# Kernel tuning notes

Hardware: AMD Instinct MI355X
Metric: run time of the kernel (lower is better)

## Reference

```python
import jax, jax.numpy as jnp
import numpy as np

N, D, IN, OUT, K = 50000, 16, 256, 128, 4  # nodes, sampled degree, input_size, output_size, heads
LEAKY_SLOPE = 0.01  # torch F.leaky_relu default


def setup_inputs() -> dict:
    key = jax.random.key(0)
    k1, k2, k3, k4 = jax.random.split(key, 4)
    X = jax.random.normal(k1, (N, IN), dtype=jnp.float32)
    W = jax.random.normal(k2, (K, OUT, IN), dtype=jnp.float32) * 0.05
    a = jax.random.normal(k3, (K, 2 * OUT), dtype=jnp.float32) * 0.05
    neighbor_idx = jax.random.randint(k4, (N, D), 0, N)  # fixed-degree neighbor sample
    return {"X": X, "W": W, "a": a, "neighbor_idx": neighbor_idx}


def reference(X, W, a, neighbor_idx):
    # X: [N, IN]; W: [K, OUT, IN]; a: [K, 2*OUT]; neighbor_idx: [N, D]
    out_dim = W.shape[1]
    # Per-head linear map of every node once: Wh[k, n] = W[k] @ X[n]
    Wh = jnp.einsum('koi,ni->kno', W, X)                       # [K, N, OUT]
    # a splits: first OUT weights multiply mapped neighbour, second OUT multiply mapped self
    a_nb, a_self = a[:, :out_dim], a[:, out_dim:]
    e_nb = jnp.einsum('kno,ko->kn', Wh, a_nb)                  # [K, N] score contribution as a neighbour
    e_self = jnp.einsum('kno,ko->kn', Wh, a_self)              # [K, N] score contribution as center node
    # Edge logits: e[k, i, d] = leaky_relu(a_nb.Wh[j] + a_self.Wh[i]), j = neighbor_idx[i, d]
    e = jax.nn.leaky_relu(e_nb[:, neighbor_idx] + e_self[:, :, None], LEAKY_SLOPE)  # [K, N, D]
    alpha = jax.nn.softmax(e, axis=-1)                         # softmax over each node's neighbour set
    Wh_nb = jnp.take(Wh, neighbor_idx, axis=1)                 # [K, N, D, OUT] gathered neighbour features
    h = jnp.einsum('knd,kndo->kno', alpha, Wh_nb)              # [K, N, OUT] attention-weighted aggregate
    # Concatenate heads along feature dim, matching per-node head-concat in the torch loop
    return jnp.transpose(h, (1, 0, 2)).reshape(X.shape[0], -1)  # [N, K*OUT]
```

## Files before the change

kernel.cpp:

```cpp
#include <hip/hip_runtime.h>

#define N_NODES 50000
#define D_NB 16
#define IN_DIM 256
#define OUT_DIM 128
#define K_HEADS 4
#define SLOPE 0.01f
#define NSLICE 16
#define SLICE_COLS 32

typedef __attribute__((ext_vector_type(8))) short short8;
typedef __attribute__((ext_vector_type(4))) float f32x4;

static __device__ __forceinline__ unsigned f2bf(float f) {
    unsigned u = __float_as_uint(f);
    unsigned r = u + 0x7fffu + ((u >> 16) & 1u);
    return r >> 16;
}
static __device__ __forceinline__ float bf2f(unsigned short b) {
    return __uint_as_float(((unsigned)b) << 16);
}

__global__ __launch_bounds__(256) void prep_w_kernel(
    const float* __restrict__ W, const float* __restrict__ a,
    unsigned short* __restrict__ Wb, float* __restrict__ wt8)
{
    if (blockIdx.x < 2048) {
        const int id = blockIdx.x * 256 + threadIdx.x;
        Wb[id] = (unsigned short)f2bf(W[id]);
        return;
    }
    const int v = blockIdx.x - 2048;
    const int k = v >> 1, s = v & 1;
    const int i = threadIdx.x;
    const float* av = a + k * 2 * OUT_DIM + s * OUT_DIM;
    float acc = 0.f;
    #pragma unroll 4
    for (int o = 0; o < OUT_DIM; ++o)
        acc += W[((size_t)k * OUT_DIM + o) * IN_DIM + i] * av[o];
    wt8[v * IN_DIM + i] = acc;
}

__global__ __launch_bounds__(256) void prep_kernel(
    const float* __restrict__ X, const float* __restrict__ wt8,
    unsigned short* __restrict__ Xb, float* __restrict__ e_nb4, float* __restrict__ e_self4)
{
    const int t = threadIdx.x;
    const int w = t >> 6;
    const int lane = t & 63;
    const int n = blockIdx.x * 4 + w;

    const f32x4 x = __builtin_nontemporal_load(
        (const f32x4*)(X + (size_t)n * IN_DIM + lane * 4));
    uint2 pk;
    pk.x = f2bf(x[0]) | (f2bf(x[1]) << 16);
    pk.y = f2bf(x[2]) | (f2bf(x[3]) << 16);
    *(uint2*)(Xb + (size_t)n * IN_DIM + lane * 4) = pk;

    float p[8];
    #pragma unroll
    for (int v = 0; v < 8; ++v) {
        const float4 wv = *(const float4*)(wt8 + v * IN_DIM + lane * 4);
        p[v] = x[0] * wv.x + x[1] * wv.y + x[2] * wv.z + x[3] * wv.w;
    }
    #pragma unroll
    for (int sh = 32; sh >= 1; sh >>= 1) {
        #pragma unroll
        for (int v = 0; v < 8; ++v) p[v] += __shfl_xor(p[v], sh);
    }
    if (lane == 0) {
        *(float4*)(e_nb4 + (size_t)n * 4)   = float4{p[0], p[2], p[4], p[6]};
        *(float4*)(e_self4 + (size_t)n * 4) = float4{p[1], p[3], p[5], p[7]};
    }
}

__global__ __launch_bounds__(256) void agg_kernel(
    const int* __restrict__ nidx, const unsigned short* __restrict__ Xb,
    const float* __restrict__ e_nb4, const float* __restrict__ e_self4,
    unsigned short* __restrict__ aggX, int n0, int nc)
{
    const int t = threadIdx.x;
    const int w = t >> 6;
    const int lane = t & 63;
    const int n = n0 + blockIdx.x * 4 + w;
    if (n >= n0 + nc || n >= N_NODES) return;

    const int k = lane >> 4;
    const int dl = lane & 15;

    const int nbr = __builtin_nontemporal_load(nidx + (size_t)n * D_NB + dl);
    const float4 eb4 = *(const float4*)(e_nb4 + (size_t)nbr * 4);
    const float4 es4 = *(const float4*)(e_self4 + (size_t)n * 4);
    const float en = (k & 2) ? ((k & 1) ? eb4.w : eb4.z) : ((k & 1) ? eb4.y : eb4.x);
    const float es = (k & 2) ? ((k & 1) ? es4.w : es4.z) : ((k & 1) ? es4.y : es4.x);
    const float xv = en + es;
    const float v = xv > 0.f ? xv : SLOPE * xv;
    float m = v;
    #pragma unroll
    for (int sh = 8; sh >= 1; sh >>= 1) m = fmaxf(m, __shfl_xor(m, sh, 16));
    const float pz = __expf(v - m);
    float sum = pz;
    #pragma unroll
    for (int sh = 8; sh >= 1; sh >>= 1) sum += __shfl_xor(sum, sh, 16);
    const float alpha = pz / sum;

    float acc[4][4] = {};
    #pragma unroll
    for (int h = 0; h < 2; ++h) {
        uint2 u[8];
        #pragma unroll
        for (int b = 0; b < 8; ++b) {
            const int nd = __shfl(nbr, h * 8 + b);
            u[b] = *(const uint2*)(Xb + (size_t)nd * IN_DIM + lane * 4);
        }
        #pragma unroll
        for (int b = 0; b < 8; ++b) {
            const float x0 = bf2f((unsigned short)(u[b].x & 0xffffu));
            const float x1 = bf2f((unsigned short)(u[b].x >> 16));
            const float x2 = bf2f((unsigned short)(u[b].y & 0xffffu));
            const float x3 = bf2f((unsigned short)(u[b].y >> 16));
            #pragma unroll
            for (int kk = 0; kk < 4; ++kk) {
                const float ad = __shfl(alpha, kk * 16 + h * 8 + b);
                acc[kk][0] += ad * x0;
                acc[kk][1] += ad * x1;
                acc[kk][2] += ad * x2;
                acc[kk][3] += ad * x3;
            }
        }
    }
    #pragma unroll
    for (int kk = 0; kk < 4; ++kk) {
        uint2 pk;
        pk.x = f2bf(acc[kk][0]) | (f2bf(acc[kk][1]) << 16);
        pk.y = f2bf(acc[kk][2]) | (f2bf(acc[kk][3]) << 16);
        *(uint2*)(aggX + ((size_t)kk * nc + (n - n0)) * IN_DIM + lane * 4) = pk;
    }
}

__global__ __launch_bounds__(512) void gemm2_kernel(
    const unsigned short* __restrict__ aggX, const unsigned short* __restrict__ Wb,
    float* __restrict__ out, int n0, int nc)
{
    __shared__ unsigned short Wlds[2][SLICE_COLS * IN_DIM];

    const int t = threadIdx.x;
    const int lane = t & 63;
    const int w = t >> 6;
    const int lrow = lane & 15;
    const int lk = lane >> 4;
    const int m0 = n0 + blockIdx.x * 256 + w * 16;

    const int arow0 = m0 + lrow;
    const int arow1 = arow0 + 128;
    const bool av0 = (arow0 < n0 + nc) && (arow0 < N_NODES);
    const bool av1 = (arow1 < n0 + nc) && (arow1 < N_NODES);

    auto STAGE = [&](int st, int buf) {
        const unsigned short* WbS = Wb + (size_t)st * SLICE_COLS * IN_DIM;
        #pragma unroll
        for (int i = 0; i < 2; ++i) {
            const int c = i * 512 + t;
            const int r = c >> 5;
            const int p = c & 31;
            const int cu = p ^ (r & 7);
            const unsigned short* gsrc = WbS + r * IN_DIM + cu * 8;
            unsigned short* ldst = &Wlds[buf][c * 8];
            __builtin_amdgcn_global_load_lds(
                (const __attribute__((address_space(1))) void*)gsrc,
                (__attribute__((address_space(3))) void*)ldst, 16, 0, 0);
        }
    };

    short8 af0[8], af1[8];
    auto LOADAF = [&](int head) {
        const size_t hb = (size_t)head * nc;
        const unsigned short* Ar0 = aggX + (hb + (arow0 - n0)) * IN_DIM + lk * 8;
        const unsigned short* Ar1 = aggX + (hb + (arow1 - n0)) * IN_DIM + lk * 8;
        #pragma unroll
        for (int kk = 0; kk < 8; ++kk) {
            af0[kk] = av0 ? *(const short8*)(Ar0 + kk * 32) : short8{0,0,0,0,0,0,0,0};
            af1[kk] = av1 ? *(const short8*)(Ar1 + kk * 32) : short8{0,0,0,0,0,0,0,0};
        }
    };

    STAGE(0, 0);
    LOADAF(0);
    __syncthreads();

    for (int st = 0; st < NSLICE; ++st) {
        const int buf = st & 1;
        if (st + 1 < NSLICE) STAGE(st + 1, buf ^ 1);
        if ((st & 3) == 0 && st) LOADAF(st >> 2);

        f32x4 acc0[2] = {}, acc1[2] = {};
        #pragma unroll
        for (int kk = 0; kk < 8; ++kk) {
            #pragma unroll
            for (int nt = 0; nt < 2; ++nt) {
                const int row = nt * 16 + lrow;
                const int pos = (kk * 4 + lk) ^ (row & 7);
                const short8 bf = *(const short8*)(&Wlds[buf][row * IN_DIM + pos * 8]);
                acc0[nt] = __builtin_amdgcn_mfma_f32_16x16x32_bf16(bf, af0[kk], acc0[nt], 0, 0, 0);
                acc1[nt] = __builtin_amdgcn_mfma_f32_16x16x32_bf16(bf, af1[kk], acc1[nt], 0, 0, 0);
            }
        }

        const int k = st >> 2, cb = st & 3;
        const size_t cbase = (size_t)k * OUT_DIM + cb * SLICE_COLS + lk * 4;
        #pragma unroll
        for (int nt = 0; nt < 2; ++nt) {
            if (av0) *(f32x4*)(out + (size_t)arow0 * (K_HEADS * OUT_DIM) + cbase + nt * 16) = acc0[nt];
            if (av1) *(f32x4*)(out + (size_t)arow1 * (K_HEADS * OUT_DIM) + cbase + nt * 16) = acc1[nt];
        }
        __syncthreads();
    }
}

extern "C" void kernel_launch(void* const* d_in, const int* in_sizes, int n_in,
                              void* d_out, int out_size, void* d_ws, size_t ws_size,
                              hipStream_t stream) {
    const float* X = (const float*)d_in[0];
    const float* W = (const float*)d_in[1];
    const float* a = (const float*)d_in[2];
    const int* nidx = (const int*)d_in[3];
    float* out = (float*)d_out;

    const size_t WbB  = (size_t)K_HEADS * OUT_DIM * IN_DIM * 2;
    const size_t XbB  = (size_t)N_NODES * IN_DIM * 2;
    const size_t wt8B = (size_t)8 * IN_DIM * 4;
    const size_t eB   = (size_t)K_HEADS * N_NODES * 4;
    auto need = [&](int nc) {
        return WbB + XbB + wt8B + 2 * eB + (size_t)K_HEADS * nc * IN_DIM * 2 + 1024;
    };

    int np, nc;
    if      (ws_size >= need(50000)) { np = 1; nc = 50000; }
    else if (ws_size >= need(25000)) { np = 2; nc = 25000; }
    else                             { np = 4; nc = 12500; }

    char* p = (char*)d_ws;
    unsigned short* Wb   = (unsigned short*)p;   p += WbB;
    unsigned short* Xb   = (unsigned short*)p;   p += XbB;
    float*          wt8  = (float*)p;            p += wt8B;
    float*          enb4 = (float*)p;            p += eB;
    float*          esf4 = (float*)p;            p += eB;
    unsigned short* aggX = (unsigned short*)p;

    hipLaunchKernelGGL(prep_w_kernel, dim3(2056), dim3(256), 0, stream, W, a, Wb, wt8);

    hipLaunchKernelGGL(prep_kernel,
        dim3(N_NODES / 4), dim3(256), 0, stream, X, wt8, Xb, enb4, esf4);

    for (int pass = 0; pass < np; ++pass) {
        const int nb0 = pass * nc;
        hipLaunchKernelGGL(agg_kernel,
            dim3((nc + 3) / 4), dim3(256), 0, stream, nidx, Xb, enb4, esf4, aggX, nb0, nc);
        hipLaunchKernelGGL(gemm2_kernel,
            dim3((nc + 255) / 256), dim3(512), 0, stream, aggX, Wb, out, nb0, nc);
    }
}
```

Measured before the change: 159.9 us.

## Fuse neighbor aggregation and per-head GEMM into one kernel via LDS tile

Merges the aggregation kernel and the GEMM kernel into a single kernel. Each block aggregates 16 nodes for all heads into a swizzled LDS tile, then runs MFMA against the bf16 weights read directly from global memory. This removes the aggX round trip through global memory, the extra kernel launch and the multi-pass workspace logic. In exchange, each block re-reads the full W slice from global memory/L2, and the agg phase and GEMM phase are serialized within a block with a barrier between them.

```diff
diff --git a/kernel.cpp b/kernel.cpp
--- a/kernel.cpp
+++ b/kernel.cpp
@@ -6,8 +6,7 @@
 #define OUT_DIM 128
 #define K_HEADS 4
 #define SLOPE 0.01f
-#define NSLICE 16
-#define SLICE_COLS 32
+#define BN 16
 
 typedef __attribute__((ext_vector_type(8))) short short8;
 typedef __attribute__((ext_vector_type(4))) float f32x4;
@@ -74,146 +73,102 @@
     }
 }
 
-__global__ __launch_bounds__(256) void agg_kernel(
+__global__ __launch_bounds__(512) void fused_kernel(
     const int* __restrict__ nidx, const unsigned short* __restrict__ Xb,
     const float* __restrict__ e_nb4, const float* __restrict__ e_self4,
-    unsigned short* __restrict__ aggX, int n0, int nc)
+    const unsigned short* __restrict__ Wb, float* __restrict__ out)
 {
+    __shared__ unsigned short tile[K_HEADS * BN * IN_DIM];
+
     const int t = threadIdx.x;
     const int w = t >> 6;
     const int lane = t & 63;
-    const int n = n0 + blockIdx.x * 4 + w;
-    if (n >= n0 + nc || n >= N_NODES) return;
+    const int bn0 = blockIdx.x * BN;
 
     const int k = lane >> 4;
     const int dl = lane & 15;
 
-    const int nbr = __builtin_nontemporal_load(nidx + (size_t)n * D_NB + dl);
-    const float4 eb4 = *(const float4*)(e_nb4 + (size_t)nbr * 4);
-    const float4 es4 = *(const float4*)(e_self4 + (size_t)n * 4);
-    const float en = (k & 2) ? ((k & 1) ? eb4.w : eb4.z) : ((k & 1) ? eb4.y : eb4.x);
-    const float es = (k & 2) ? ((k & 1) ? es4.w : es4.z) : ((k & 1) ? es4.y : es4.x);
-    const float xv = en + es;
-    const float v = xv > 0.f ? xv : SLOPE * xv;
-    float m = v;
     #pragma unroll
-    for (int sh = 8; sh >= 1; sh >>= 1) m = fmaxf(m, __shfl_xor(m, sh, 16));
-    const float pz = __expf(v - m);
-    float sum = pz;
-    #pragma unroll
-    for (int sh = 8; sh >= 1; sh >>= 1) sum += __shfl_xor(sum, sh, 16);
-    const float alpha = pz / sum;
+    for (int half = 0; half < 2; ++half) {
+        const int row = 2 * w + half;
+        const int n = bn0 + row;
 
-    float acc[4][4] = {};
-    #pragma unroll
-    for (int h = 0; h < 2; ++h) {
-        uint2 u[8];
+        const int nbr = __builtin_nontemporal_load(nidx + (size_t)n * D_NB + dl);
+        const float4 eb4 = *(const float4*)(e_nb4 + (size_t)nbr * 4);
+        const float4 es4 = *(const float4*)(e_self4 + (size_t)n * 4);
+        const float en = (k & 2) ? ((k & 1) ? eb4.w : eb4.z) : ((k & 1) ? eb4.y : eb4.x);
+        const float es = (k & 2) ? ((k & 1) ? es4.w : es4.z) : ((k & 1) ? es4.y : es4.x);
+        const float xv = en + es;
+        const float v = xv > 0.f ? xv : SLOPE * xv;
+        float m = v;
         #pragma unroll
-        for (int b = 0; b < 8; ++b) {
-            const int nd = __shfl(nbr, h * 8 + b);
-            u[b] = *(const uint2*)(Xb + (size_t)nd * IN_DIM + lane * 4);
+        for (int sh = 8; sh >= 1; sh >>= 1) m = fmaxf(m, __shfl_xor(m, sh, 16));
+        const float pz = __expf(v - m);
+        float sum = pz;
+        #pragma unroll
+        for (int sh = 8; sh >= 1; sh >>= 1) sum += __shfl_xor(sum, sh, 16);
+        const float alpha = pz / sum;
+
+        float acc[4][4] = {};
+        #pragma unroll
+        for (int h2 = 0; h2 < 2; ++h2) {
+            uint2 u[8];
+            #pragma unroll
+            for (int b = 0; b < 8; ++b) {
+                const int nd = __shfl(nbr, h2 * 8 + b);
+                u[b] = *(const uint2*)(Xb + (size_t)nd * IN_DIM + lane * 4);
+            }
+            #pragma unroll
+            for (int b = 0; b < 8; ++b) {
+                const float x0 = bf2f((unsigned short)(u[b].x & 0xffffu));
+                const float x1 = bf2f((unsigned short)(u[b].x >> 16));
+                const float x2 = bf2f((unsigned short)(u[b].y & 0xffffu));
+                const float x3 = bf2f((unsigned short)(u[b].y >> 16));
+                #pragma unroll
+                for (int kk = 0; kk < 4; ++kk) {
+                    const float ad = __shfl(alpha, kk * 16 + h2 * 8 + b);
+                    acc[kk][0] += ad * x0;
+                    acc[kk][1] += ad * x1;
+                    acc[kk][2] += ad * x2;
+                    acc[kk][3] += ad * x3;
+                }
+            }
         }
         #pragma unroll
-        for (int b = 0; b < 8; ++b) {
-            const float x0 = bf2f((unsigned short)(u[b].x & 0xffffu));
-            const float x1 = bf2f((unsigned short)(u[b].x >> 16));
-            const float x2 = bf2f((unsigned short)(u[b].y & 0xffffu));
-            const float x3 = bf2f((unsigned short)(u[b].y >> 16));
-            #pragma unroll
-            for (int kk = 0; kk < 4; ++kk) {
-                const float ad = __shfl(alpha, kk * 16 + h * 8 + b);
-                acc[kk][0] += ad * x0;
-                acc[kk][1] += ad * x1;
-                acc[kk][2] += ad * x2;
-                acc[kk][3] += ad * x3;
-            }
+        for (int kk = 0; kk < 4; ++kk) {
+            uint2 pk;
+            pk.x = f2bf(acc[kk][0]) | (f2bf(acc[kk][1]) << 16);
+            pk.y = f2bf(acc[kk][2]) | (f2bf(acc[kk][3]) << 16);
+            const int boff = (kk * (BN * IN_DIM * 2) + row * (IN_DIM * 2) + lane * 8)
+                             ^ ((row & 7) << 4);
+            *(uint2*)((char*)tile + boff) = pk;
+        }
+    }
+    __syncthreads();
+
+    const int h = w >> 1;
+    const int c4 = (w & 1) * 4;
+    const int lrow = lane & 15;
+    const int lk = lane >> 4;
+
+    f32x4 acc2[4] = {};
+    #pragma unroll
+    for (int kk = 0; kk < 8; ++kk) {
+        const int aoff = (h * (BN * IN_DIM * 2) + lrow * (IN_DIM * 2) + kk * 64 + lk * 16)
+                         ^ ((lrow & 7) << 4);
+        const short8 af = *(const short8*)((const char*)tile + aoff);
+        #pragma unroll
+        for (int c = 0; c < 4; ++c) {
+            const int ocol = (c4 + c) * 16 + lrow;
+            const short8 bf = *(const short8*)(
+                Wb + ((size_t)h * OUT_DIM + ocol) * IN_DIM + kk * 32 + lk * 8);
+            acc2[c] = __builtin_amdgcn_mfma_f32_16x16x32_bf16(bf, af, acc2[c], 0, 0, 0);
         }
     }
     #pragma unroll
-    for (int kk = 0; kk < 4; ++kk) {
-        uint2 pk;
-        pk.x = f2bf(acc[kk][0]) | (f2bf(acc[kk][1]) << 16);
-        pk.y = f2bf(acc[kk][2]) | (f2bf(acc[kk][3]) << 16);
-        *(uint2*)(aggX + ((size_t)kk * nc + (n - n0)) * IN_DIM + lane * 4) = pk;
-    }
-}
-
-__global__ __launch_bounds__(512) void gemm2_kernel(
-    const unsigned short* __restrict__ aggX, const unsigned short* __restrict__ Wb,
-    float* __restrict__ out, int n0, int nc)
-{
-    __shared__ unsigned short Wlds[2][SLICE_COLS * IN_DIM];
-
-    const int t = threadIdx.x;
-    const int lane = t & 63;
-    const int w = t >> 6;
-    const int lrow = lane & 15;
-    const int lk = lane >> 4;
-    const int m0 = n0 + blockIdx.x * 256 + w * 16;
-
-    const int arow0 = m0 + lrow;
-    const int arow1 = arow0 + 128;
-    const bool av0 = (arow0 < n0 + nc) && (arow0 < N_NODES);
-    const bool av1 = (arow1 < n0 + nc) && (arow1 < N_NODES);
-
-    auto STAGE = [&](int st, int buf) {
-        const unsigned short* WbS = Wb + (size_t)st * SLICE_COLS * IN_DIM;
-        #pragma unroll
-        for (int i = 0; i < 2; ++i) {
-            const int c = i * 512 + t;
-            const int r = c >> 5;
-            const int p = c & 31;
-            const int cu = p ^ (r & 7);
-            const unsigned short* gsrc = WbS + r * IN_DIM + cu * 8;
-            unsigned short* ldst = &Wlds[buf][c * 8];
-            __builtin_amdgcn_global_load_lds(
-                (const __attribute__((address_space(1))) void*)gsrc,
-                (__attribute__((address_space(3))) void*)ldst, 16, 0, 0);
-        }
-    };
-
-    short8 af0[8], af1[8];
-    auto LOADAF = [&](int head) {
-        const size_t hb = (size_t)head * nc;
-        const unsigned short* Ar0 = aggX + (hb + (arow0 - n0)) * IN_DIM + lk * 8;
-        const unsigned short* Ar1 = aggX + (hb + (arow1 - n0)) * IN_DIM + lk * 8;
-        #pragma unroll
-        for (int kk = 0; kk < 8; ++kk) {
-            af0[kk] = av0 ? *(const short8*)(Ar0 + kk * 32) : short8{0,0,0,0,0,0,0,0};
-            af1[kk] = av1 ? *(const short8*)(Ar1 + kk * 32) : short8{0,0,0,0,0,0,0,0};
-        }
-    };
-
-    STAGE(0, 0);
-    LOADAF(0);
-    __syncthreads();
-
-    for (int st = 0; st < NSLICE; ++st) {
-        const int buf = st & 1;
-        if (st + 1 < NSLICE) STAGE(st + 1, buf ^ 1);
-        if ((st & 3) == 0 && st) LOADAF(st >> 2);
-
-        f32x4 acc0[2] = {}, acc1[2] = {};
-        #pragma unroll
-        for (int kk = 0; kk < 8; ++kk) {
-            #pragma unroll
-            for (int nt = 0; nt < 2; ++nt) {
-                const int row = nt * 16 + lrow;
-                const int pos = (kk * 4 + lk) ^ (row & 7);
-                const short8 bf = *(const short8*)(&Wlds[buf][row * IN_DIM + pos * 8]);
-                acc0[nt] = __builtin_amdgcn_mfma_f32_16x16x32_bf16(bf, af0[kk], acc0[nt], 0, 0, 0);
-                acc1[nt] = __builtin_amdgcn_mfma_f32_16x16x32_bf16(bf, af1[kk], acc1[nt], 0, 0, 0);
-            }
-        }
-
-        const int k = st >> 2, cb = st & 3;
-        const size_t cbase = (size_t)k * OUT_DIM + cb * SLICE_COLS + lk * 4;
-        #pragma unroll
-        for (int nt = 0; nt < 2; ++nt) {
-            if (av0) *(f32x4*)(out + (size_t)arow0 * (K_HEADS * OUT_DIM) + cbase + nt * 16) = acc0[nt];
-            if (av1) *(f32x4*)(out + (size_t)arow1 * (K_HEADS * OUT_DIM) + cbase + nt * 16) = acc1[nt];
-        }
-        __syncthreads();
+    for (int c = 0; c < 4; ++c) {
+        *(f32x4*)(out + (size_t)(bn0 + lrow) * (K_HEADS * OUT_DIM)
+                  + h * OUT_DIM + (c4 + c) * 16 + lk * 4) = acc2[c];
     }
 }
 
@@ -226,37 +181,18 @@
     const int* nidx = (const int*)d_in[3];
     float* out = (float*)d_out;
 
-    const size_t WbB  = (size_t)K_HEADS * OUT_DIM * IN_DIM * 2;
-    const size_t XbB  = (size_t)N_NODES * IN_DIM * 2;
-    const size_t wt8B = (size_t)8 * IN_DIM * 4;
-    const size_t eB   = (size_t)K_HEADS * N_NODES * 4;
-    auto need = [&](int nc) {
-        return WbB + XbB + wt8B + 2 * eB + (size_t)K_HEADS * nc * IN_DIM * 2 + 1024;
-    };
-
-    int np, nc;
-    if      (ws_size >= need(50000)) { np = 1; nc = 50000; }
-    else if (ws_size >= need(25000)) { np = 2; nc = 25000; }
-    else                             { np = 4; nc = 12500; }
-
     char* p = (char*)d_ws;
-    unsigned short* Wb   = (unsigned short*)p;   p += WbB;
-    unsigned short* Xb   = (unsigned short*)p;   p += XbB;
-    float*          wt8  = (float*)p;            p += wt8B;
-    float*          enb4 = (float*)p;            p += eB;
-    float*          esf4 = (float*)p;            p += eB;
-    unsigned short* aggX = (unsigned short*)p;
+    unsigned short* Wb   = (unsigned short*)p;   p += (size_t)K_HEADS * OUT_DIM * IN_DIM * 2;
+    unsigned short* Xb   = (unsigned short*)p;   p += (size_t)N_NODES * IN_DIM * 2;
+    float*          wt8  = (float*)p;            p += (size_t)8 * IN_DIM * 4;
+    float*          enb4 = (float*)p;            p += (size_t)K_HEADS * N_NODES * 4;
+    float*          esf4 = (float*)p;
 
     hipLaunchKernelGGL(prep_w_kernel, dim3(2056), dim3(256), 0, stream, W, a, Wb, wt8);
 
     hipLaunchKernelGGL(prep_kernel,
         dim3(N_NODES / 4), dim3(256), 0, stream, X, wt8, Xb, enb4, esf4);
 
-    for (int pass = 0; pass < np; ++pass) {
-        const int nb0 = pass * nc;
-        hipLaunchKernelGGL(agg_kernel,
-            dim3((nc + 3) / 4), dim3(256), 0, stream, nidx, Xb, enb4, esf4, aggX, nb0, nc);
-        hipLaunchKernelGGL(gemm2_kernel,
-            dim3((nc + 255) / 256), dim3(512), 0, stream, aggX, Wb, out, nb0, nc);
-    }
+    hipLaunchKernelGGL(fused_kernel,
+        dim3(N_NODES / BN), dim3(512), 0, stream, nidx, Xb, enb4, esf4, Wb, out);
 }
```

After: 206.7 us. +29.3%, slower.
